# Kernel tuning notes

Measured on AMD Instinct MI355X. Metric: run time of the kernel, lower is better.

## Reference

```python
import jax, jax.numpy as jnp
import numpy as np

N_CLASS = 8192
FEAT_DIM = 1024
BATCH = 1024
PROTO_M = 0.95
TEMP = 0.1
BASE_TEMP = 0.1
EPS = 1e-12  # F.normalize eps


def setup_inputs() -> dict:
    key = jax.random.key(0)
    k1, k2, k3 = jax.random.split(key, 3)
    features = jax.random.normal(k1, (BATCH, FEAT_DIM), dtype=jnp.float32)
    labels = jax.random.randint(k2, (BATCH,), 0, N_CLASS)
    prototypes = jax.random.normal(k3, (N_CLASS, FEAT_DIM), dtype=jnp.float32)
    # init_class_prototypes ends with F.normalize(prototypes, dim=1)
    prototypes = prototypes / jnp.maximum(
        jnp.linalg.norm(prototypes, axis=1, keepdims=True), EPS)
    return {"features": features, "labels": labels, "prototypes": prototypes}


def _ema_update(prototypes, features, labels):
    # Sequential per-sample EMA scatter update (order matters for repeated labels),
    # expressed as a lax.scan over the batch.
    def step(protos, fl):
        f, l = fl
        row = protos[l] * PROTO_M + f * (1.0 - PROTO_M)
        row = row / jnp.maximum(jnp.linalg.norm(row), EPS)  # F.normalize(dim=0)
        return protos.at[l].set(row), None

    protos, _ = jax.lax.scan(step, prototypes, (features, labels))
    return protos


def reference(features, labels, prototypes):
    protos = _ema_update(prototypes, features, labels)  # [C, D]
    logits = jnp.matmul(protos, protos.T) / TEMP        # [C, C]
    exp_l = jnp.exp(logits)
    # mask = off-diagonal ones (labels are arange(n_class)), so the masked sum
    # is the row sum minus the diagonal; mask.sum(1) == n_class - 1 (never NaN).
    sum_neg = exp_l.sum(axis=1) - jnp.diagonal(exp_l)   # [C]
    mean_prob_neg = jnp.log(sum_neg / jnp.float32(N_CLASS - 1))
    loss = (TEMP / BASE_TEMP) * jnp.mean(mean_prob_neg)
    return loss
```

## Files before the change

### kernel.cpp

```cpp
#include <hip/hip_runtime.h>
#include <math.h>

#define C 8192
#define D 1024
#define BATCH 1024
#define PM 0.95f
#define PMC 0.05f
#define INVT_SCALED 0.15625f

typedef unsigned char u8;
typedef __attribute__((ext_vector_type(16))) float f32x16;

#define GLOBAL_AS(p) ((const __attribute__((address_space(1))) void*)(p))
#define LDS_AS(p) ((__attribute__((address_space(3))) void*)(p))

__global__ __launch_bounds__(256) void ema_split_kernel(const float* __restrict__ feat,
                                                        const int* __restrict__ labels,
                                                        const float* __restrict__ protos,
                                                        u8* __restrict__ P8,
                                                        float* __restrict__ rowsum,
                                                        float* __restrict__ out) {
    __shared__ int sl[BATCH];
    __shared__ unsigned int sq[128][16][2];
    const int t = threadIdx.x, w = t >> 6, lane = t & 63;
    const int cb = blockIdx.x * 16;

    if (blockIdx.x < 32) rowsum[blockIdx.x * 256 + t] = 0.0f;
    if (blockIdx.x == 0 && t == 0) out[0] = 0.0f;

    for (int i = t; i < BATCH; i += 256) sl[i] = labels[i];
    __syncthreads();

    for (int i = 0; i < 4; ++i) {
        const int c = cb + w * 4 + i;

        float4 v[4];
        #pragma unroll
        for (int s = 0; s < 4; ++s)
            v[s] = *(const float4*)(protos + (size_t)c * D + s * 256 + lane * 4);

        for (int base = 0; base < BATCH; base += 64) {
            unsigned long long mask = __ballot(sl[base + lane] == c);
            while (mask) {
                const int b = __ffsll((long long)mask) - 1;
                mask &= mask - 1;
                const int idx = base + b;
                float ss = 0.0f;
                #pragma unroll
                for (int s = 0; s < 4; ++s) {
                    const float4 f = *(const float4*)(feat + (size_t)idx * D + s * 256 + lane * 4);
                    v[s].x = v[s].x * PM + f.x * PMC;
                    v[s].y = v[s].y * PM + f.y * PMC;
                    v[s].z = v[s].z * PM + f.z * PMC;
                    v[s].w = v[s].w * PM + f.w * PMC;
                    ss += v[s].x * v[s].x + v[s].y * v[s].y + v[s].z * v[s].z + v[s].w * v[s].w;
                }
                #pragma unroll
                for (int off = 32; off > 0; off >>= 1) ss += __shfl_xor(ss, off);
                const float inv = 1.0f / fmaxf(sqrtf(ss), 1e-12f);
                #pragma unroll
                for (int s = 0; s < 4; ++s) {
                    v[s].x *= inv; v[s].y *= inv; v[s].z *= inv; v[s].w *= inv;
                }
            }
        }

        #pragma unroll
        for (int s = 0; s < 4; ++s) {
            int p = __builtin_amdgcn_cvt_pk_fp8_f32(v[s].x * 8.0f, v[s].y * 8.0f, 0, false);
            p = __builtin_amdgcn_cvt_pk_fp8_f32(v[s].z * 8.0f, v[s].w * 8.0f, p, true);
            sq[s * 32 + (lane >> 1)][w * 4 + i][lane & 1] = (unsigned int)p;
        }
    }
    __syncthreads();

    u8* base = P8 + (size_t)(cb >> 5) * 32768 + (cb & 31) * 8;
    #pragma unroll
    for (int it = 0; it < 4; ++it) {
        const int slot = it * 256 + t;
        const int pp = slot >> 3, a = slot & 7;
        uint4 val;
        val.x = sq[pp][2 * a][0];     val.y = sq[pp][2 * a][1];
        val.z = sq[pp][2 * a + 1][0]; val.w = sq[pp][2 * a + 1][1];
        *(uint4*)(base + (pp >> 1) * 512 + (pp & 1) * 256 + a * 16) = val;
    }
}

__global__ __launch_bounds__(256, 4) void gram8_kernel(const u8* __restrict__ P8,
                                                       float* __restrict__ rowsum) {
    __shared__ u8 lds[5][8192];
    const int t = threadIdx.x, w = t >> 6, lane = t & 63;

    int mm = blockIdx.x >> 3;
    const int r = blockIdx.x & 7;
    int bi = 0;
    #pragma unroll
    for (int s = 0; s < 8; ++s) {
        const int strip = (s & 1) ? ((s >> 1) * 16 + 15 - r) : ((s >> 1) * 16 + r);
        const int n = 64 - strip;
        if (mm < n) { bi = strip; break; }
        mm -= n;
    }
    const int bj = bi + mm;
    const bool diag = (bi == bj);

    const u8* gsrcA = P8 + (size_t)(bi * 4 + w) * 32768 + lane * 16;
    const u8* gsrcB = P8 + (size_t)(bj * 4 + w) * 32768 + lane * 16;
    const int ldsA = w * 1024, ldsB = 4096 + w * 1024;

    const int qi = w >> 1, qj = w & 1;
    const int aoff = qi * 2048 + lane * 8;
    const int boff = 4096 + qj * 2048 + lane * 8;

    f32x16 acc[2][2];
    #pragma unroll
    for (int a = 0; a < 2; ++a)
        #pragma unroll
        for (int b = 0; b < 2; ++b)
            #pragma unroll
            for (int e = 0; e < 16; ++e) acc[a][b][e] = 0.0f;

    long fa[2][2], fb[2][2];

#define STAGE(KC, BUF)                                                         \
    __builtin_amdgcn_global_load_lds(GLOBAL_AS(gsrcA + (size_t)(KC) * 1024),   \
                                     LDS_AS(&lds[BUF][ldsA]), 16, 0, 0);       \
    __builtin_amdgcn_global_load_lds(GLOBAL_AS(gsrcB + (size_t)(KC) * 1024),   \
                                     LDS_AS(&lds[BUF][ldsB]), 16, 0, 0);

#define PF(SET, BUF, KK)                                                       \
    fa[SET][0] = *(const long*)&lds[BUF][aoff + (KK) * 512];                   \
    fa[SET][1] = *(const long*)&lds[BUF][aoff + 1024 + (KK) * 512];            \
    fb[SET][0] = *(const long*)&lds[BUF][boff + (KK) * 512];                   \
    fb[SET][1] = *(const long*)&lds[BUF][boff + 1024 + (KK) * 512];

#define MFMA4(SET)                                                             \
    acc[0][0] = __builtin_amdgcn_mfma_f32_32x32x16_fp8_fp8(fa[SET][0], fb[SET][0], acc[0][0], 0, 0, 0); \
    acc[0][1] = __builtin_amdgcn_mfma_f32_32x32x16_fp8_fp8(fa[SET][0], fb[SET][1], acc[0][1], 0, 0, 0); \
    acc[1][0] = __builtin_amdgcn_mfma_f32_32x32x16_fp8_fp8(fa[SET][1], fb[SET][0], acc[1][0], 0, 0, 0); \
    acc[1][1] = __builtin_amdgcn_mfma_f32_32x32x16_fp8_fp8(fa[SET][1], fb[SET][1], acc[1][1], 0, 0, 0);

#define WAITV(N) asm volatile("s_waitcnt vmcnt(" #N ")" ::: "memory")

    STAGE(0, 0); STAGE(1, 1); STAGE(2, 2); STAGE(3, 3);
    WAITV(4);
    __builtin_amdgcn_s_barrier();
    PF(0, 0, 0);

    int cb = 0;
    for (int kc = 0; kc < 28; ++kc) {
        const int sb = (cb >= 1) ? cb - 1 : 4;
        STAGE(kc + 4, sb);
        const int nb = (cb == 4) ? 0 : cb + 1;
        PF(1, cb, 1);
        MFMA4(0);
        PF(0, nb, 0);
        MFMA4(1);
        WAITV(4);
        __builtin_amdgcn_s_barrier();
        cb = nb;
    }
    PF(1, 3, 1); MFMA4(0);
    PF(0, 4, 0); MFMA4(1);
    WAITV(2); __builtin_amdgcn_s_barrier();
    PF(1, 4, 1); MFMA4(0);
    PF(0, 0, 0); MFMA4(1);
    WAITV(0); __builtin_amdgcn_s_barrier();
    PF(1, 0, 1); MFMA4(0);
    PF(0, 1, 0); MFMA4(1);
    PF(1, 1, 1); MFMA4(0);
    MFMA4(1);

    __syncthreads();
    float* rpart = (float*)&lds[0][0];
    float* cpart = (float*)&lds[0][512];
    if (t < 128) { rpart[t] = 0.0f; cpart[t] = 0.0f; }
    __syncthreads();
    const int half = lane >> 5, col = lane & 31;
    float csum[2] = {0.0f, 0.0f};
    #pragma unroll
    for (int ti = 0; ti < 2; ++ti) {
        float rs[16];
        #pragma unroll
        for (int reg = 0; reg < 16; ++reg) rs[reg] = 0.0f;
        #pragma unroll
        for (int tj = 0; tj < 2; ++tj) {
            const int lj = qj * 64 + tj * 32 + col;
            #pragma unroll
            for (int reg = 0; reg < 16; ++reg) {
                const int li = qi * 64 + ti * 32 + (reg & 3) + 8 * (reg >> 2) + 4 * half;
                float e = __expf(acc[ti][tj][reg] * INVT_SCALED);
                if (diag && li >= lj) e = 0.0f;
                rs[reg] += e;
                csum[tj] += e;
            }
        }
        #pragma unroll
        for (int reg = 0; reg < 16; ++reg) {
            float v = rs[reg];
            v += __shfl_xor(v, 1); v += __shfl_xor(v, 2); v += __shfl_xor(v, 4);
            v += __shfl_xor(v, 8); v += __shfl_xor(v, 16);
            if (col == 0)
                atomicAdd(&rpart[qi * 64 + ti * 32 + (reg & 3) + 8 * (reg >> 2) + 4 * half], v);
        }
    }
    #pragma unroll
    for (int tj = 0; tj < 2; ++tj) {
        float v = csum[tj];
        v += __shfl_xor(v, 32);
        if (half == 0) atomicAdd(&cpart[qj * 64 + tj * 32 + col], v);
    }
    __syncthreads();
    if (t < 128) atomicAdd(&rowsum[bi * 128 + t], rpart[t]);
    else         atomicAdd(&rowsum[bj * 128 + (t - 128)], cpart[t - 128]);
}

__global__ __launch_bounds__(256) void final2_kernel(const float* __restrict__ rowsum,
                                                     float* __restrict__ out) {
    __shared__ float red[4];
    const int t = threadIdx.x;
    const int i = blockIdx.x * 256 + t;
    float v = logf(rowsum[i] * (1.0f / (float)(C - 1)));
    #pragma unroll
    for (int off = 32; off > 0; off >>= 1) v += __shfl_down(v, off);
    if ((t & 63) == 0) red[t >> 6] = v;
    __syncthreads();
    if (t == 0)
        atomicAdd(out, (red[0] + red[1] + red[2] + red[3]) * (1.0f / (float)C));
}

extern "C" void kernel_launch(void* const* d_in, const int* in_sizes, int n_in,
                              void* d_out, int out_size, void* d_ws, size_t ws_size,
                              hipStream_t stream) {
    const float* feat = (const float*)d_in[0];
    const int* labels = (const int*)d_in[1];
    const float* protos = (const float*)d_in[2];
    float* out = (float*)d_out;
    float* rowsum = (float*)d_ws;
    u8* P8 = (u8*)((char*)d_ws + 32768);

    ema_split_kernel<<<C / 16, 256, 0, stream>>>(feat, labels, protos, P8, rowsum, out);
    gram8_kernel<<<2080, 256, 0, stream>>>(P8, rowsum);
    final2_kernel<<<C / 256, 256, 0, stream>>>(rowsum, out);
}
```

Baseline: 151.2 us.

## Use two waves per gram block with 64x128 warp tiles

```diff
diff --git a/kernel.cpp b/kernel.cpp
--- a/kernel.cpp
+++ b/kernel.cpp
@@ -86,10 +86,10 @@
     }
 }
 
-__global__ __launch_bounds__(256, 4) void gram8_kernel(const u8* __restrict__ P8,
+__global__ __launch_bounds__(128, 2) void gram8_kernel(const u8* __restrict__ P8,
                                                        float* __restrict__ rowsum) {
     __shared__ u8 lds[5][8192];
-    const int t = threadIdx.x, w = t >> 6, lane = t & 63;
+    const int t = threadIdx.x, w2 = t >> 6, lane = t & 63;
 
     int mm = blockIdx.x >> 3;
     const int r = blockIdx.x & 7;
@@ -104,91 +104,96 @@
     const int bj = bi + mm;
     const bool diag = (bi == bj);
 
-    const u8* gsrcA = P8 + (size_t)(bi * 4 + w) * 32768 + lane * 16;
-    const u8* gsrcB = P8 + (size_t)(bj * 4 + w) * 32768 + lane * 16;
-    const int ldsA = w * 1024, ldsB = 4096 + w * 1024;
-
-    const int qi = w >> 1, qj = w & 1;
-    const int aoff = qi * 2048 + lane * 8;
-    const int boff = 4096 + qj * 2048 + lane * 8;
-
-    f32x16 acc[2][2];
+    const u8* gA = P8 + (size_t)(bi * 4 + 2 * w2) * 32768 + lane * 16;
+    const u8* gB = P8 + (size_t)(bj * 4 + 2 * w2) * 32768 + lane * 16;
+    const int ldsA = 2 * w2 * 1024, ldsB = 4096 + 2 * w2 * 1024;
+
+    const int aoff = w2 * 2048 + lane * 8;
+    const int boff = 4096 + lane * 8;
+
+    f32x16 acc[2][4];
     #pragma unroll
     for (int a = 0; a < 2; ++a)
         #pragma unroll
-        for (int b = 0; b < 2; ++b)
+        for (int b = 0; b < 4; ++b)
             #pragma unroll
             for (int e = 0; e < 16; ++e) acc[a][b][e] = 0.0f;
 
-    long fa[2][2], fb[2][2];
-
 #define STAGE(KC, BUF)                                                         \
-    __builtin_amdgcn_global_load_lds(GLOBAL_AS(gsrcA + (size_t)(KC) * 1024),   \
+    __builtin_amdgcn_global_load_lds(GLOBAL_AS(gA + (size_t)(KC) * 1024),      \
                                      LDS_AS(&lds[BUF][ldsA]), 16, 0, 0);       \
-    __builtin_amdgcn_global_load_lds(GLOBAL_AS(gsrcB + (size_t)(KC) * 1024),   \
-                                     LDS_AS(&lds[BUF][ldsB]), 16, 0, 0);
-
-#define PF(SET, BUF, KK)                                                       \
-    fa[SET][0] = *(const long*)&lds[BUF][aoff + (KK) * 512];                   \
-    fa[SET][1] = *(const long*)&lds[BUF][aoff + 1024 + (KK) * 512];            \
-    fb[SET][0] = *(const long*)&lds[BUF][boff + (KK) * 512];                   \
-    fb[SET][1] = *(const long*)&lds[BUF][boff + 1024 + (KK) * 512];
-
-#define MFMA4(SET)                                                             \
-    acc[0][0] = __builtin_amdgcn_mfma_f32_32x32x16_fp8_fp8(fa[SET][0], fb[SET][0], acc[0][0], 0, 0, 0); \
-    acc[0][1] = __builtin_amdgcn_mfma_f32_32x32x16_fp8_fp8(fa[SET][0], fb[SET][1], acc[0][1], 0, 0, 0); \
-    acc[1][0] = __builtin_amdgcn_mfma_f32_32x32x16_fp8_fp8(fa[SET][1], fb[SET][0], acc[1][0], 0, 0, 0); \
-    acc[1][1] = __builtin_amdgcn_mfma_f32_32x32x16_fp8_fp8(fa[SET][1], fb[SET][1], acc[1][1], 0, 0, 0);
+    __builtin_amdgcn_global_load_lds(GLOBAL_AS(gA + (size_t)(KC) * 1024 + 32768), \
+                                     LDS_AS(&lds[BUF][ldsA + 1024]), 16, 0, 0);   \
+    __builtin_amdgcn_global_load_lds(GLOBAL_AS(gB + (size_t)(KC) * 1024),      \
+                                     LDS_AS(&lds[BUF][ldsB]), 16, 0, 0);       \
+    __builtin_amdgcn_global_load_lds(GLOBAL_AS(gB + (size_t)(KC) * 1024 + 32768), \
+                                     LDS_AS(&lds[BUF][ldsB + 1024]), 16, 0, 0);
+
+#define CHUNK(BUF)                                                             \
+    {                                                                          \
+        long fa0[2], fb0[4], fa1[2], fb1[4];                                   \
+        fa0[0] = *(const long*)&lds[BUF][aoff];                                \
+        fa0[1] = *(const long*)&lds[BUF][aoff + 1024];                         \
+        fb0[0] = *(const long*)&lds[BUF][boff];                                \
+        fb0[1] = *(const long*)&lds[BUF][boff + 1024];                         \
+        fb0[2] = *(const long*)&lds[BUF][boff + 2048];                         \
+        fb0[3] = *(const long*)&lds[BUF][boff + 3072];                         \
+        fa1[0] = *(const long*)&lds[BUF][aoff + 512];                          \
+        fa1[1] = *(const long*)&lds[BUF][aoff + 1536];                         \
+        fb1[0] = *(const long*)&lds[BUF][boff + 512];                          \
+        fb1[1] = *(const long*)&lds[BUF][boff + 1536];                         \
+        fb1[2] = *(const long*)&lds[BUF][boff + 2560];                         \
+        fb1[3] = *(const long*)&lds[BUF][boff + 3584];                         \
+        _Pragma("unroll")                                                      \
+        for (int j = 0; j < 4; ++j) {                                          \
+            acc[0][j] = __builtin_amdgcn_mfma_f32_32x32x16_fp8_fp8(fa0[0], fb0[j], acc[0][j], 0, 0, 0); \
+            acc[1][j] = __builtin_amdgcn_mfma_f32_32x32x16_fp8_fp8(fa0[1], fb0[j], acc[1][j], 0, 0, 0); \
+        }                                                                      \
+        _Pragma("unroll")                                                      \
+        for (int j = 0; j < 4; ++j) {                                          \
+            acc[0][j] = __builtin_amdgcn_mfma_f32_32x32x16_fp8_fp8(fa1[0], fb1[j], acc[0][j], 0, 0, 0); \
+            acc[1][j] = __builtin_amdgcn_mfma_f32_32x32x16_fp8_fp8(fa1[1], fb1[j], acc[1][j], 0, 0, 0); \
+        }                                                                      \
+    }
 
 #define WAITV(N) asm volatile("s_waitcnt vmcnt(" #N ")" ::: "memory")
 
     STAGE(0, 0); STAGE(1, 1); STAGE(2, 2); STAGE(3, 3);
-    WAITV(4);
+    WAITV(12);
     __builtin_amdgcn_s_barrier();
-    PF(0, 0, 0);
 
     int cb = 0;
     for (int kc = 0; kc < 28; ++kc) {
         const int sb = (cb >= 1) ? cb - 1 : 4;
         STAGE(kc + 4, sb);
-        const int nb = (cb == 4) ? 0 : cb + 1;
-        PF(1, cb, 1);
-        MFMA4(0);
-        PF(0, nb, 0);
-        MFMA4(1);
-        WAITV(4);
+        CHUNK(cb);
+        WAITV(12);
         __builtin_amdgcn_s_barrier();
-        cb = nb;
-    }
-    PF(1, 3, 1); MFMA4(0);
-    PF(0, 4, 0); MFMA4(1);
-    WAITV(2); __builtin_amdgcn_s_barrier();
-    PF(1, 4, 1); MFMA4(0);
-    PF(0, 0, 0); MFMA4(1);
-    WAITV(0); __builtin_amdgcn_s_barrier();
-    PF(1, 0, 1); MFMA4(0);
-    PF(0, 1, 0); MFMA4(1);
-    PF(1, 1, 1); MFMA4(0);
-    MFMA4(1);
+        cb = (cb == 4) ? 0 : cb + 1;
+    }
+    CHUNK(3); WAITV(8);  __builtin_amdgcn_s_barrier();
+    CHUNK(4); WAITV(4);  __builtin_amdgcn_s_barrier();
+    CHUNK(0); WAITV(0);  __builtin_amdgcn_s_barrier();
+    CHUNK(1);
 
     __syncthreads();
     float* rpart = (float*)&lds[0][0];
     float* cpart = (float*)&lds[0][512];
-    if (t < 128) { rpart[t] = 0.0f; cpart[t] = 0.0f; }
+    rpart[t] = 0.0f; cpart[t] = 0.0f;
     __syncthreads();
     const int half = lane >> 5, col = lane & 31;
-    float csum[2] = {0.0f, 0.0f};
+    float csum[4] = {0.0f, 0.0f, 0.0f, 0.0f};
     #pragma unroll
     for (int ti = 0; ti < 2; ++ti) {
         float rs[16];
         #pragma unroll
         for (int reg = 0; reg < 16; ++reg) rs[reg] = 0.0f;
         #pragma unroll
-        for (int tj = 0; tj < 2; ++tj) {
-            const int lj = qj * 64 + tj * 32 + col;
+        for (int tj = 0; tj < 4; ++tj) {
+            const int lj = tj * 32 + col;
             #pragma unroll
             for (int reg = 0; reg < 16; ++reg) {
-                const int li = qi * 64 + ti * 32 + (reg & 3) + 8 * (reg >> 2) + 4 * half;
+                const int li = w2 * 64 + ti * 32 + (reg & 3) + 8 * (reg >> 2) + 4 * half;
                 float e = __expf(acc[ti][tj][reg] * INVT_SCALED);
                 if (diag && li >= lj) e = 0.0f;
                 rs[reg] += e;
@@ -201,18 +206,18 @@
             v += __shfl_xor(v, 1); v += __shfl_xor(v, 2); v += __shfl_xor(v, 4);
             v += __shfl_xor(v, 8); v += __shfl_xor(v, 16);
             if (col == 0)
-                atomicAdd(&rpart[qi * 64 + ti * 32 + (reg & 3) + 8 * (reg >> 2) + 4 * half], v);
-        }
-    }
-    #pragma unroll
-    for (int tj = 0; tj < 2; ++tj) {
+                atomicAdd(&rpart[w2 * 64 + ti * 32 + (reg & 3) + 8 * (reg >> 2) + 4 * half], v);
+        }
+    }
+    #pragma unroll
+    for (int tj = 0; tj < 4; ++tj) {
         float v = csum[tj];
         v += __shfl_xor(v, 32);
-        if (half == 0) atomicAdd(&cpart[qj * 64 + tj * 32 + col], v);
-    }
-    __syncthreads();
-    if (t < 128) atomicAdd(&rowsum[bi * 128 + t], rpart[t]);
-    else         atomicAdd(&rowsum[bj * 128 + (t - 128)], cpart[t - 128]);
+        if (half == 0) atomicAdd(&cpart[tj * 32 + col], v);
+    }
+    __syncthreads();
+    atomicAdd(&rowsum[bi * 128 + t], rpart[t]);
+    atomicAdd(&rowsum[bj * 128 + t], cpart[t]);
 }
 
 __global__ __launch_bounds__(256) void final2_kernel(const float* __restrict__ rowsum,
@@ -240,6 +245,6 @@
     u8* P8 = (u8*)((char*)d_ws + 32768);
 
     ema_split_kernel<<<C / 16, 256, 0, stream>>>(feat, labels, protos, P8, rowsum, out);
-    gram8_kernel<<<2080, 256, 0, stream>>>(P8, rowsum);
+    gram8_kernel<<<2080, 128, 0, stream>>>(P8, rowsum);
     final2_kernel<<<C / 256, 256, 0, stream>>>(rowsum, out);
 }
```

After: 160.8 us. +6.4%, slower.

## Switch Gram GEMM to scaled 32x32x64 FP8 MFMA with two-chunk pipeline

Applied to the files above, without the earlier changes.

```diff
diff --git a/kernel.cpp b/kernel.cpp
--- a/kernel.cpp
+++ b/kernel.cpp
@@ -10,6 +10,7 @@
 
 typedef unsigned char u8;
 typedef __attribute__((ext_vector_type(16))) float f32x16;
+typedef __attribute__((ext_vector_type(8))) int i32x8;
 
 #define GLOBAL_AS(p) ((const __attribute__((address_space(1))) void*)(p))
 #define LDS_AS(p) ((__attribute__((address_space(3))) void*)(p))
@@ -109,8 +110,9 @@
     const int ldsA = w * 1024, ldsB = 4096 + w * 1024;
 
     const int qi = w >> 1, qj = w & 1;
-    const int aoff = qi * 2048 + lane * 8;
-    const int boff = 4096 + qj * 2048 + lane * 8;
+    const int aT0 = qi * 2048, aT1 = qi * 2048 + 1024;
+    const int bT0 = 4096 + qj * 2048, bT1 = 4096 + qj * 2048 + 1024;
+    const int cb8 = (lane & 31) * 8;
 
     f32x16 acc[2][2];
     #pragma unroll
@@ -119,8 +121,6 @@
         for (int b = 0; b < 2; ++b)
             #pragma unroll
             for (int e = 0; e < 16; ++e) acc[a][b][e] = 0.0f;
-
-    long fa[2][2], fb[2][2];
 
 #define STAGE(KC, BUF)                                                         \
     __builtin_amdgcn_global_load_lds(GLOBAL_AS(gsrcA + (size_t)(KC) * 1024),   \
@@ -128,48 +128,55 @@
     __builtin_amdgcn_global_load_lds(GLOBAL_AS(gsrcB + (size_t)(KC) * 1024),   \
                                      LDS_AS(&lds[BUF][ldsB]), 16, 0, 0);
 
-#define PF(SET, BUF, KK)                                                       \
-    fa[SET][0] = *(const long*)&lds[BUF][aoff + (KK) * 512];                   \
-    fa[SET][1] = *(const long*)&lds[BUF][aoff + 1024 + (KK) * 512];            \
-    fb[SET][0] = *(const long*)&lds[BUF][boff + (KK) * 512];                   \
-    fb[SET][1] = *(const long*)&lds[BUF][boff + 1024 + (KK) * 512];
-
-#define MFMA4(SET)                                                             \
-    acc[0][0] = __builtin_amdgcn_mfma_f32_32x32x16_fp8_fp8(fa[SET][0], fb[SET][0], acc[0][0], 0, 0, 0); \
-    acc[0][1] = __builtin_amdgcn_mfma_f32_32x32x16_fp8_fp8(fa[SET][0], fb[SET][1], acc[0][1], 0, 0, 0); \
-    acc[1][0] = __builtin_amdgcn_mfma_f32_32x32x16_fp8_fp8(fa[SET][1], fb[SET][0], acc[1][0], 0, 0, 0); \
-    acc[1][1] = __builtin_amdgcn_mfma_f32_32x32x16_fp8_fp8(fa[SET][1], fb[SET][1], acc[1][1], 0, 0, 0);
+#define LD8(DST, HB, TB)                                                       \
+    {                                                                          \
+        long* P_ = (long*)&(DST);                                              \
+        P_[0] = *(const long*)((HB) + (TB) + cb8);                             \
+        P_[1] = *(const long*)((HB) + (TB) + cb8 + 256);                       \
+        P_[2] = *(const long*)((HB) + (TB) + cb8 + 512);                       \
+        P_[3] = *(const long*)((HB) + (TB) + cb8 + 768);                       \
+    }
+
+#define CHUNK2(C0, C1)                                                         \
+    {                                                                          \
+        const u8* hb = (lane & 32) ? &lds[C1][0] : &lds[C0][0];                \
+        i32x8 va0, va1, vb0, vb1;                                              \
+        LD8(va0, hb, aT0); LD8(va1, hb, aT1);                                  \
+        LD8(vb0, hb, bT0); LD8(vb1, hb, bT1);                                  \
+        acc[0][0] = __builtin_amdgcn_mfma_scale_f32_32x32x64_f8f6f4(           \
+            va0, vb0, acc[0][0], 0, 0, 0, 0x7F7F7F7F, 0, 0x7F7F7F7F);          \
+        acc[0][1] = __builtin_amdgcn_mfma_scale_f32_32x32x64_f8f6f4(           \
+            va0, vb1, acc[0][1], 0, 0, 0, 0x7F7F7F7F, 0, 0x7F7F7F7F);          \
+        acc[1][0] = __builtin_amdgcn_mfma_scale_f32_32x32x64_f8f6f4(           \
+            va1, vb0, acc[1][0], 0, 0, 0, 0x7F7F7F7F, 0, 0x7F7F7F7F);          \
+        acc[1][1] = __builtin_amdgcn_mfma_scale_f32_32x32x64_f8f6f4(           \
+            va1, vb1, acc[1][1], 0, 0, 0, 0x7F7F7F7F, 0, 0x7F7F7F7F);          \
+    }
 
 #define WAITV(N) asm volatile("s_waitcnt vmcnt(" #N ")" ::: "memory")
 
-    STAGE(0, 0); STAGE(1, 1); STAGE(2, 2); STAGE(3, 3);
-    WAITV(4);
+    STAGE(0, 0); STAGE(1, 1); STAGE(2, 2);
+    WAITV(2);
     __builtin_amdgcn_s_barrier();
-    PF(0, 0, 0);
-
-    int cb = 0;
-    for (int kc = 0; kc < 28; ++kc) {
-        const int sb = (cb >= 1) ? cb - 1 : 4;
-        STAGE(kc + 4, sb);
-        const int nb = (cb == 4) ? 0 : cb + 1;
-        PF(1, cb, 1);
-        MFMA4(0);
-        PF(0, nb, 0);
-        MFMA4(1);
-        WAITV(4);
+
+    int c0 = 0;
+    for (int p = 0; p < 14; ++p) {
+        const int c1  = (c0 == 4) ? 0 : c0 + 1;
+        const int nc0 = (c1 == 4) ? 0 : c1 + 1;
+        const int s0  = (nc0 == 4) ? 0 : nc0 + 1;
+        const int s1  = (s0 == 4) ? 0 : s0 + 1;
+        STAGE(2 * p + 3, s0);
+        STAGE(2 * p + 4, s1);
+        CHUNK2(c0, c1);
+        WAITV(2);
         __builtin_amdgcn_s_barrier();
-        cb = nb;
-    }
-    PF(1, 3, 1); MFMA4(0);
-    PF(0, 4, 0); MFMA4(1);
-    WAITV(2); __builtin_amdgcn_s_barrier();
-    PF(1, 4, 1); MFMA4(0);
-    PF(0, 0, 0); MFMA4(1);
-    WAITV(0); __builtin_amdgcn_s_barrier();
-    PF(1, 0, 1); MFMA4(0);
-    PF(0, 1, 0); MFMA4(1);
-    PF(1, 1, 1); MFMA4(0);
-    MFMA4(1);
+        c0 = nc0;
+    }
+    STAGE(31, 1);
+    CHUNK2(3, 4);
+    WAITV(0);
+    __builtin_amdgcn_s_barrier();
+    CHUNK2(0, 1);
 
     __syncthreads();
     float* rpart = (float*)&lds[0][0];
```

Measured after the change: 406.4 us. 2.69x slower.

## Switch prototype Gram matrix from FP8 to INT8 MFMA with symmetric scaling

Applied to the files above, without the earlier changes.

```diff
diff --git a/kernel.cpp b/kernel.cpp
--- a/kernel.cpp
+++ b/kernel.cpp
@@ -6,10 +6,11 @@
 #define BATCH 1024
 #define PM 0.95f
 #define PMC 0.05f
-#define INVT_SCALED 0.15625f
+#define INVT_I8 (10.0f / 16129.0f)
 
 typedef unsigned char u8;
-typedef __attribute__((ext_vector_type(16))) float f32x16;
+typedef __attribute__((ext_vector_type(16))) int i32x16;
+typedef __attribute__((ext_vector_type(4))) int i32x4;
 
 #define GLOBAL_AS(p) ((const __attribute__((address_space(1))) void*)(p))
 #define LDS_AS(p) ((__attribute__((address_space(3))) void*)(p))
@@ -21,7 +22,7 @@
                                                         float* __restrict__ rowsum,
                                                         float* __restrict__ out) {
     __shared__ int sl[BATCH];
-    __shared__ unsigned int sq[128][16][2];
+    __shared__ unsigned int sq[64][16][4];
     const int t = threadIdx.x, w = t >> 6, lane = t & 63;
     const int cb = blockIdx.x * 16;
 
@@ -67,22 +68,26 @@
 
         #pragma unroll
         for (int s = 0; s < 4; ++s) {
-            int p = __builtin_amdgcn_cvt_pk_fp8_f32(v[s].x * 8.0f, v[s].y * 8.0f, 0, false);
-            p = __builtin_amdgcn_cvt_pk_fp8_f32(v[s].z * 8.0f, v[s].w * 8.0f, p, true);
-            sq[s * 32 + (lane >> 1)][w * 4 + i][lane & 1] = (unsigned int)p;
-        }
-    }
-    __syncthreads();
-
-    u8* base = P8 + (size_t)(cb >> 5) * 32768 + (cb & 31) * 8;
+            const int qx = __float2int_rn(v[s].x * 127.0f);
+            const int qy = __float2int_rn(v[s].y * 127.0f);
+            const int qz = __float2int_rn(v[s].z * 127.0f);
+            const int qw = __float2int_rn(v[s].w * 127.0f);
+            const unsigned int pk = (qx & 0xFF) | ((qy & 0xFF) << 8) |
+                                    ((qz & 0xFF) << 16) | ((unsigned int)(qw & 0xFF) << 24);
+            sq[s * 16 + (lane >> 2)][w * 4 + i][lane & 3] = pk;
+        }
+    }
+    __syncthreads();
+
+    u8* base2 = P8 + (size_t)(cb >> 5) * 32768 + (cb & 31) * 16;
     #pragma unroll
     for (int it = 0; it < 4; ++it) {
         const int slot = it * 256 + t;
-        const int pp = slot >> 3, a = slot & 7;
+        const int pp16 = slot >> 4, cls = slot & 15;
         uint4 val;
-        val.x = sq[pp][2 * a][0];     val.y = sq[pp][2 * a][1];
-        val.z = sq[pp][2 * a + 1][0]; val.w = sq[pp][2 * a + 1][1];
-        *(uint4*)(base + (pp >> 1) * 512 + (pp & 1) * 256 + a * 16) = val;
+        val.x = sq[pp16][cls][0]; val.y = sq[pp16][cls][1];
+        val.z = sq[pp16][cls][2]; val.w = sq[pp16][cls][3];
+        *(uint4*)(base2 + (pp16 >> 1) * 1024 + (pp16 & 1) * 512 + cls * 16) = val;
     }
 }
 
@@ -109,18 +114,19 @@
     const int ldsA = w * 1024, ldsB = 4096 + w * 1024;
 
     const int qi = w >> 1, qj = w & 1;
-    const int aoff = qi * 2048 + lane * 8;
-    const int boff = 4096 + qj * 2048 + lane * 8;
-
-    f32x16 acc[2][2];
+    const int aT0 = qi * 2048;
+    const int bT0 = 4096 + qj * 2048;
+    const int alof = (lane >> 5) * 512 + (lane & 31) * 16;
+
+    i32x16 acc[2][2];
     #pragma unroll
     for (int a = 0; a < 2; ++a)
         #pragma unroll
         for (int b = 0; b < 2; ++b)
             #pragma unroll
-            for (int e = 0; e < 16; ++e) acc[a][b][e] = 0.0f;
-
-    long fa[2][2], fb[2][2];
+            for (int e = 0; e < 16; ++e) acc[a][b][e] = 0;
+
+    i32x4 fa[2][2], fb[2][2];
 
 #define STAGE(KC, BUF)                                                         \
     __builtin_amdgcn_global_load_lds(GLOBAL_AS(gsrcA + (size_t)(KC) * 1024),   \
@@ -128,47 +134,44 @@
     __builtin_amdgcn_global_load_lds(GLOBAL_AS(gsrcB + (size_t)(KC) * 1024),   \
                                      LDS_AS(&lds[BUF][ldsB]), 16, 0, 0);
 
-#define PF(SET, BUF, KK)                                                       \
-    fa[SET][0] = *(const long*)&lds[BUF][aoff + (KK) * 512];                   \
-    fa[SET][1] = *(const long*)&lds[BUF][aoff + 1024 + (KK) * 512];            \
-    fb[SET][0] = *(const long*)&lds[BUF][boff + (KK) * 512];                   \
-    fb[SET][1] = *(const long*)&lds[BUF][boff + 1024 + (KK) * 512];
+#define PF(SET, BUF)                                                           \
+    fa[SET][0] = *(const i32x4*)&lds[BUF][aT0 + alof];                         \
+    fa[SET][1] = *(const i32x4*)&lds[BUF][aT0 + 1024 + alof];                  \
+    fb[SET][0] = *(const i32x4*)&lds[BUF][bT0 + alof];                         \
+    fb[SET][1] = *(const i32x4*)&lds[BUF][bT0 + 1024 + alof];
 
 #define MFMA4(SET)                                                             \
-    acc[0][0] = __builtin_amdgcn_mfma_f32_32x32x16_fp8_fp8(fa[SET][0], fb[SET][0], acc[0][0], 0, 0, 0); \
-    acc[0][1] = __builtin_amdgcn_mfma_f32_32x32x16_fp8_fp8(fa[SET][0], fb[SET][1], acc[0][1], 0, 0, 0); \
-    acc[1][0] = __builtin_amdgcn_mfma_f32_32x32x16_fp8_fp8(fa[SET][1], fb[SET][0], acc[1][0], 0, 0, 0); \
-    acc[1][1] = __builtin_amdgcn_mfma_f32_32x32x16_fp8_fp8(fa[SET][1], fb[SET][1], acc[1][1], 0, 0, 0);
+    acc[0][0] = __builtin_amdgcn_mfma_i32_32x32x32_i8(fa[SET][0], fb[SET][0], acc[0][0], 0, 0, 0); \
+    acc[0][1] = __builtin_amdgcn_mfma_i32_32x32x32_i8(fa[SET][0], fb[SET][1], acc[0][1], 0, 0, 0); \
+    acc[1][0] = __builtin_amdgcn_mfma_i32_32x32x32_i8(fa[SET][1], fb[SET][0], acc[1][0], 0, 0, 0); \
+    acc[1][1] = __builtin_amdgcn_mfma_i32_32x32x32_i8(fa[SET][1], fb[SET][1], acc[1][1], 0, 0, 0);
 
 #define WAITV(N) asm volatile("s_waitcnt vmcnt(" #N ")" ::: "memory")
 
     STAGE(0, 0); STAGE(1, 1); STAGE(2, 2); STAGE(3, 3);
     WAITV(4);
     __builtin_amdgcn_s_barrier();
-    PF(0, 0, 0);
-
-    int cb = 0;
+    PF(0, 0);
+
+    int cbuf = 0;
     for (int kc = 0; kc < 28; ++kc) {
-        const int sb = (cb >= 1) ? cb - 1 : 4;
+        const int sb = (cbuf >= 1) ? cbuf - 1 : 4;
         STAGE(kc + 4, sb);
-        const int nb = (cb == 4) ? 0 : cb + 1;
-        PF(1, cb, 1);
-        MFMA4(0);
-        PF(0, nb, 0);
-        MFMA4(1);
+        const int nb = (cbuf == 4) ? 0 : cbuf + 1;
+        PF((kc + 1) & 1, nb);
+        MFMA4(kc & 1);
         WAITV(4);
         __builtin_amdgcn_s_barrier();
-        cb = nb;
-    }
-    PF(1, 3, 1); MFMA4(0);
-    PF(0, 4, 0); MFMA4(1);
+        cbuf = nb;
+    }
+    PF(1, 4);
+    MFMA4(0);
     WAITV(2); __builtin_amdgcn_s_barrier();
-    PF(1, 4, 1); MFMA4(0);
-    PF(0, 0, 0); MFMA4(1);
+    PF(0, 0);
+    MFMA4(1);
     WAITV(0); __builtin_amdgcn_s_barrier();
-    PF(1, 0, 1); MFMA4(0);
-    PF(0, 1, 0); MFMA4(1);
-    PF(1, 1, 1); MFMA4(0);
+    PF(1, 1);
+    MFMA4(0);
     MFMA4(1);
 
     __syncthreads();
@@ -189,7 +192,7 @@
             #pragma unroll
             for (int reg = 0; reg < 16; ++reg) {
                 const int li = qi * 64 + ti * 32 + (reg & 3) + 8 * (reg >> 2) + 4 * half;
-                float e = __expf(acc[ti][tj][reg] * INVT_SCALED);
+                float e = __expf((float)acc[ti][tj][reg] * INVT_I8);
                 if (diag && li >= lj) e = 0.0f;
                 rs[reg] += e;
                 csum[tj] += e;
```

Result: faster. 147.7 us (median of 4 runs) (-2.3%).
